# Performance work log

Measured on AMD Instinct MI355X. Metric: run time of the kernel, lower is better.

## Reference

```python
import jax, jax.numpy as jnp
import numpy as np

B_, L_, D_, N_ = 4, 4096, 64, 16
DT = 0.1
EPS = 1e-6


def _complex_log(x):
    # log|x| (clamped) + i*pi for negative entries, matching torch impl
    real = jnp.log(jnp.maximum(jnp.abs(x), EPS))
    imag = jnp.where(x < 0, jnp.float32(np.pi), jnp.float32(0.0))
    return jax.lax.complex(real, imag)


def _clogaddexp(a, b):
    # stable complex log(exp(a)+exp(b)) using max of real parts
    m = jnp.maximum(a.real, b.real)
    return jnp.log(jnp.exp(a - m) + jnp.exp(b - m)) + m


def _clogcumsumexp(x, axis):
    return jax.lax.associative_scan(_clogaddexp, x, axis=axis)


def setup_inputs() -> dict:
    key = jax.random.key(0)
    ks = jax.random.split(key, 6)
    x = jax.random.normal(ks[0], (B_, L_, D_), jnp.float32)
    s = 1.0 / np.sqrt(D_)
    Wb = jax.random.uniform(ks[1], (N_, D_), jnp.float32, -s, s)
    bb = jax.random.uniform(ks[2], (N_,), jnp.float32, -s, s)
    Wc = jax.random.uniform(ks[3], (N_, D_), jnp.float32, -s, s)
    bc = jax.random.uniform(ks[4], (N_,), jnp.float32, -s, s)
    Wd = jax.random.uniform(ks[5], (1, D_), jnp.float32, -s, s)
    bd = jnp.zeros((1,), jnp.float32)
    # S4D-Real init: A_n = -(n+1), repeated over input_dim rows -> (D, N)
    A = jnp.tile(-(jnp.arange(N_, dtype=jnp.float32) + 1.0)[None, :], (D_, 1))
    return {"x": x, "A": A, "Wb": Wb, "bb": bb, "Wc": Wc, "bc": bc,
            "Wd": Wd, "bd": bd}


def reference(x, A, Wb, bb, Wc, bc, Wd, bd):
    # projections: (b,l,n)
    Bm = x @ Wb.T + bb
    Cm = x @ Wc.T + bc
    # delta network: softplus(linear(x)) + dt, broadcast to input_dim
    delta = jax.nn.softplus(x @ Wd.T + bd) + DT            # (b,l,1)
    dt = jnp.broadcast_to(delta, x.shape)                  # (b,l,d)
    # discretize
    tmp = A * dt[..., None]                                # (b,l,d,n)
    A_bar = jnp.exp(tmp)
    delta_B = jnp.einsum('bld,bln->bldn', dt, Bm)
    B_bar = (A_bar - 1.0) * delta_B / (tmp + EPS)
    term2 = B_bar * x[..., None]                           # (b,l,d,n)
    # parallel scan via complex log-cumsum-exp trick
    log_a = _complex_log(A_bar)
    log_b = _complex_log(term2)
    a_star = jnp.cumsum(log_a, axis=1)                     # (b,l,d,n) complex
    t = _clogcumsumexp(log_b - a_star, axis=1)
    scan = jnp.exp(a_star + t).real                        # (b,l,d,n)
    return jnp.sum(scan * Cm[:, :, None, :], axis=-1)      # (b,l,d)
```

## Files before the change

### kernel.cpp

```cpp
#include <hip/hip_runtime.h>

#define B_ 4
#define L_ 4096
#define D_ 64
#define N_ 16
#define CHUNK 16
#define NCHUNK (L_ / CHUNK)
#define TOTCHUNK (B_ * NCHUNK)

constexpr float DT_  = 0.1f;
constexpr float EPS_ = 1e-6f;

__global__ __launch_bounds__(64) void proj_scan_kernel(
    const float* __restrict__ x,  const float* __restrict__ A,
    const float* __restrict__ Wb, const float* __restrict__ bb,
    const float* __restrict__ Wc, const float* __restrict__ bc,
    const float* __restrict__ Wd, const float* __restrict__ bd,
    float* __restrict__ S, float* __restrict__ Cdec,
    float* __restrict__ Wcor, float* __restrict__ out)
{
    const int gc    = blockIdx.x;
    const int batch = gc >> 8;
    const int c     = gc & (NCHUNK - 1);
    const int lane  = threadIdx.x;
    const int base0 = batch * L_ + c * CHUNK;

    __shared__ float xs[CHUNK * D_];
    __shared__ float ag[CHUNK * 32];
    __shared__ float cm[CHUNK * N_];
    __shared__ float wbuf[CHUNK * N_];

    const float4* xg  = (const float4*)(x + (size_t)base0 * D_);
    float4*       xsv = (float4*)xs;
    #pragma unroll
    for (int i = 0; i < 4; i++) xsv[i * 64 + lane] = xg[i * 64 + lane];

    const int o  = lane & 31;
    const int h2 = lane >> 5;
    float wreg[32];
    const float* Wrow = (o < 16) ? (Wb + o * D_) : (Wc + (o - 16) * D_);
    const float4* w4p = (const float4*)(Wrow + h2 * 32);
    #pragma unroll
    for (int j = 0; j < 8; j++) {
        float4 w4 = w4p[j];
        wreg[4*j+0] = w4.x; wreg[4*j+1] = w4.y;
        wreg[4*j+2] = w4.z; wreg[4*j+3] = w4.w;
    }
    const float wd   = Wd[lane];
    const float bd0  = bd[0];
    const float An   = A[lane & 15];
    const float bias = (o < 16) ? bb[o] : bc[o - 16];

    __syncthreads();

    float r[CHUNK];
    #pragma unroll
    for (int p = 0; p < CHUNK; p++) r[p] = xs[p * D_ + lane] * wd;
    #pragma unroll
    for (int m = 32; m >= 1; m >>= 1) {
        #pragma unroll
        for (int p = 0; p < CHUNK; p++) r[p] += __shfl_xor(r[p], m, 64);
    }
    float delta[CHUNK];
    #pragma unroll
    for (int p = 0; p < CHUNK; p++) {
        float z = r[p] + bd0;
        delta[p] = fmaxf(z, 0.0f) + log1pf(expf(-fabsf(z))) + DT_;
    }

    #pragma unroll
    for (int p = 0; p < CHUNK; p++) {
        float acc = 0.0f;
        const float4* xs4 = (const float4*)(xs + p * D_ + h2 * 32);
        #pragma unroll
        for (int j = 0; j < 8; j++) {
            float4 v = xs4[j];
            acc += v.x * wreg[4*j+0] + v.y * wreg[4*j+1]
                 + v.z * wreg[4*j+2] + v.w * wreg[4*j+3];
        }
        acc += __shfl_xor(acc, 32, 64);
        if (lane < 16) {
            float Bm  = acc + bias;
            float tmp = An * delta[p];
            float a   = expf(tmp);
            float g   = (a - 1.0f) * delta[p] * Bm / (tmp + EPS_);
            ag[p * 32 + lane]      = a;
            ag[p * 32 + 16 + lane] = g;
        } else if (lane < 32) {
            cm[p * 16 + (lane - 16)] = acc + bias;
        }
    }
    __syncthreads();

    float h[N_];
    #pragma unroll
    for (int n = 0; n < N_; n++) h[n] = 0.0f;
    for (int s = 0; s < CHUNK; s++) {
        float xd = xs[s * D_ + lane];
        const float4* row = (const float4*)(ag + s * 32);
        const float4* crw = (const float4*)(cm + s * 16);
        float acc = 0.0f;
        #pragma unroll
        for (int q = 0; q < 4; q++) {
            float4 a4 = row[q];
            float4 g4 = row[4 + q];
            float4 c4 = crw[q];
            h[4*q+0] = a4.x * h[4*q+0] + g4.x * xd;  acc += c4.x * h[4*q+0];
            h[4*q+1] = a4.y * h[4*q+1] + g4.y * xd;  acc += c4.y * h[4*q+1];
            h[4*q+2] = a4.z * h[4*q+2] + g4.z * xd;  acc += c4.z * h[4*q+2];
            h[4*q+3] = a4.w * h[4*q+3] + g4.w * xd;  acc += c4.w * h[4*q+3];
        }
        out[(size_t)(base0 + s) * D_ + lane] = acc;
    }
    #pragma unroll
    for (int n = 0; n < N_; n++)
        S[(size_t)(gc * N_ + n) * D_ + lane] = h[n];

    if (lane < 16) {
        float cumn = 1.0f;
        for (int s = 0; s < CHUNK; s++) {
            cumn *= ag[s * 32 + lane];
            wbuf[s * 16 + lane] = cm[s * 16 + lane] * cumn;
        }
        Cdec[gc * N_ + lane] = cumn;
    }
    __syncthreads();
    ((float4*)(Wcor + (size_t)base0 * 16))[lane] = ((const float4*)wbuf)[lane];
}

#define G_ 32
__global__ __launch_bounds__(64) void combine(
    float* __restrict__ S, const float* __restrict__ Cdec)
{
    const int b = blockIdx.x >> 4;
    const int n = blockIdx.x & 15;
    const int d = threadIdx.x;
    const int cb = b * NCHUNK;

    float*       baseS = S    + (size_t)(cb * N_ + n) * D_ + d;
    const float* baseA = Cdec + cb * N_ + n;

    float run = 0.0f;
    float sbuf[G_], abuf[G_];
    #pragma unroll
    for (int j = 0; j < G_; j++) {
        sbuf[j] = baseS[(size_t)j * (N_ * D_)];
        abuf[j] = baseA[j * N_];
    }
    for (int cc = 0; cc < NCHUNK; cc += G_) {
        const int cn = (cc + G_ < NCHUNK) ? (cc + G_) : cc;
        float t[G_], u[G_];
        #pragma unroll
        for (int j = 0; j < G_; j++) {
            t[j] = baseS[(size_t)(cn + j) * (N_ * D_)];
            u[j] = baseA[(cn + j) * N_];
        }
        #pragma unroll
        for (int j = 0; j < G_; j++) {
            baseS[(size_t)(cc + j) * (N_ * D_)] = run;
            run = abuf[j] * run + sbuf[j];
        }
        #pragma unroll
        for (int j = 0; j < G_; j++) { sbuf[j] = t[j]; abuf[j] = u[j]; }
    }
}

__global__ __launch_bounds__(64) void apply_kernel(
    const float* __restrict__ Wcor, const float* __restrict__ S,
    float* __restrict__ out)
{
    const int gc    = blockIdx.x;
    const int batch = gc >> 8;
    const int c     = gc & (NCHUNK - 1);
    const int lane  = threadIdx.x;
    const int base0 = batch * L_ + c * CHUNK;

    __shared__ float wl[CHUNK * N_];

    ((float4*)wl)[lane] = ((const float4*)(Wcor + (size_t)base0 * 16))[lane];

    float hi[N_];
    #pragma unroll
    for (int n = 0; n < N_; n++)
        hi[n] = S[(size_t)(gc * N_ + n) * D_ + lane];

    float4 ov[4];
    const float4* og = (const float4*)(out + (size_t)base0 * D_);
    #pragma unroll
    for (int i = 0; i < 4; i++) ov[i] = og[i * 64 + lane];

    __syncthreads();

    float acc[CHUNK];
    #pragma unroll
    for (int s = 0; s < CHUNK; s++) {
        const float4* crw = (const float4*)(wl + s * 16);
        float a = 0.0f;
        #pragma unroll
        for (int q = 0; q < 4; q++) {
            float4 w4 = crw[q];
            a += w4.x * hi[4*q+0] + w4.y * hi[4*q+1]
               + w4.z * hi[4*q+2] + w4.w * hi[4*q+3];
        }
        acc[s] = a;
    }

    #pragma unroll
    for (int s = 0; s < CHUNK; s++)
        out[(size_t)(base0 + s) * D_ + lane] = out[(size_t)(base0 + s) * D_ + lane] + acc[s];
}

extern "C" void kernel_launch(void* const* d_in, const int* in_sizes, int n_in,
                              void* d_out, int out_size, void* d_ws, size_t ws_size,
                              hipStream_t stream)
{
    const float* x  = (const float*)d_in[0];
    const float* A  = (const float*)d_in[1];
    const float* Wb = (const float*)d_in[2];
    const float* bb = (const float*)d_in[3];
    const float* Wc = (const float*)d_in[4];
    const float* bc = (const float*)d_in[5];
    const float* Wd = (const float*)d_in[6];
    const float* bd = (const float*)d_in[7];
    float* out = (float*)d_out;

    float* S    = (float*)d_ws;
    float* Cdec = S    + (size_t)TOTCHUNK * N_ * D_;
    float* Wcor = Cdec + (size_t)TOTCHUNK * N_;

    proj_scan_kernel<<<TOTCHUNK, 64, 0, stream>>>(x, A, Wb, bb, Wc, bc, Wd, bd,
                                                  S, Cdec, Wcor, out);
    combine<<<B_ * N_, 64, 0, stream>>>(S, Cdec);
    apply_kernel<<<TOTCHUNK, 64, 0, stream>>>(Wcor, S, out);
}
```

Before: 104.5 us.

## Split chunk work across four wavefronts per block in scan and apply kernels

Both per-chunk kernels now launch 256 threads instead of 64. In the projection/scan kernel each wavefront handles four timesteps of the projection and four of the sixteen state dimensions in the intra-chunk recurrence. Per-wave partial outputs are reduced through a new shared-memory buffer. The apply kernel also spreads timesteps across waves and folds the existing output into its accumulator. The aim is more parallelism and shorter serial chains per thread, which should help latency hiding with only 1024 blocks, at the cost of extra shared memory and a reduction pass.

New measurement: 100.3 us. 4.1% less time.

```diff
diff --git a/kernel.cpp b/kernel.cpp
--- a/kernel.cpp
+++ b/kernel.cpp
@@ -11,7 +11,7 @@
 constexpr float DT_  = 0.1f;
 constexpr float EPS_ = 1e-6f;
 
-__global__ __launch_bounds__(64) void proj_scan_kernel(
+__global__ __launch_bounds__(256) void proj_scan_kernel(
     const float* __restrict__ x,  const float* __restrict__ A,
     const float* __restrict__ Wb, const float* __restrict__ bb,
     const float* __restrict__ Wc, const float* __restrict__ bc,
@@ -22,18 +22,18 @@
     const int gc    = blockIdx.x;
     const int batch = gc >> 8;
     const int c     = gc & (NCHUNK - 1);
-    const int lane  = threadIdx.x;
+    const int tid   = threadIdx.x;
+    const int w     = tid >> 6;
+    const int lane  = tid & 63;
     const int base0 = batch * L_ + c * CHUNK;
 
     __shared__ float xs[CHUNK * D_];
     __shared__ float ag[CHUNK * 32];
     __shared__ float cm[CHUNK * N_];
     __shared__ float wbuf[CHUNK * N_];
-
-    const float4* xg  = (const float4*)(x + (size_t)base0 * D_);
-    float4*       xsv = (float4*)xs;
-    #pragma unroll
-    for (int i = 0; i < 4; i++) xsv[i * 64 + lane] = xg[i * 64 + lane];
+    __shared__ float pout[4 * CHUNK * D_];
+
+    ((float4*)xs)[tid] = ((const float4*)(x + (size_t)base0 * D_))[tid];
 
     const int o  = lane & 31;
     const int h2 = lane >> 5;
@@ -53,25 +53,27 @@
 
     __syncthreads();
 
-    float r[CHUNK];
-    #pragma unroll
-    for (int p = 0; p < CHUNK; p++) r[p] = xs[p * D_ + lane] * wd;
+    const int s0 = w * 4;
+    float r[4];
+    #pragma unroll
+    for (int p = 0; p < 4; p++) r[p] = xs[(s0 + p) * D_ + lane] * wd;
     #pragma unroll
     for (int m = 32; m >= 1; m >>= 1) {
         #pragma unroll
-        for (int p = 0; p < CHUNK; p++) r[p] += __shfl_xor(r[p], m, 64);
-    }
-    float delta[CHUNK];
-    #pragma unroll
-    for (int p = 0; p < CHUNK; p++) {
+        for (int p = 0; p < 4; p++) r[p] += __shfl_xor(r[p], m, 64);
+    }
+    float delta[4];
+    #pragma unroll
+    for (int p = 0; p < 4; p++) {
         float z = r[p] + bd0;
         delta[p] = fmaxf(z, 0.0f) + log1pf(expf(-fabsf(z))) + DT_;
     }
 
     #pragma unroll
-    for (int p = 0; p < CHUNK; p++) {
+    for (int p = 0; p < 4; p++) {
+        const int s = s0 + p;
         float acc = 0.0f;
-        const float4* xs4 = (const float4*)(xs + p * D_ + h2 * 32);
+        const float4* xs4 = (const float4*)(xs + s * D_ + h2 * 32);
         #pragma unroll
         for (int j = 0; j < 8; j++) {
             float4 v = xs4[j];
@@ -84,48 +86,53 @@
             float tmp = An * delta[p];
             float a   = expf(tmp);
             float g   = (a - 1.0f) * delta[p] * Bm / (tmp + EPS_);
-            ag[p * 32 + lane]      = a;
-            ag[p * 32 + 16 + lane] = g;
+            ag[s * 32 + lane]      = a;
+            ag[s * 32 + 16 + lane] = g;
         } else if (lane < 32) {
-            cm[p * 16 + (lane - 16)] = acc + bias;
-        }
-    }
-    __syncthreads();
-
-    float h[N_];
-    #pragma unroll
-    for (int n = 0; n < N_; n++) h[n] = 0.0f;
+            cm[s * 16 + (lane - 16)] = acc + bias;
+        }
+    }
+    __syncthreads();
+
+    const int n0 = w * 4;
+    float h0 = 0.0f, h1 = 0.0f, h2v = 0.0f, h3 = 0.0f;
+    #pragma unroll
     for (int s = 0; s < CHUNK; s++) {
-        float xd = xs[s * D_ + lane];
-        const float4* row = (const float4*)(ag + s * 32);
-        const float4* crw = (const float4*)(cm + s * 16);
-        float acc = 0.0f;
-        #pragma unroll
-        for (int q = 0; q < 4; q++) {
-            float4 a4 = row[q];
-            float4 g4 = row[4 + q];
-            float4 c4 = crw[q];
-            h[4*q+0] = a4.x * h[4*q+0] + g4.x * xd;  acc += c4.x * h[4*q+0];
-            h[4*q+1] = a4.y * h[4*q+1] + g4.y * xd;  acc += c4.y * h[4*q+1];
-            h[4*q+2] = a4.z * h[4*q+2] + g4.z * xd;  acc += c4.z * h[4*q+2];
-            h[4*q+3] = a4.w * h[4*q+3] + g4.w * xd;  acc += c4.w * h[4*q+3];
-        }
-        out[(size_t)(base0 + s) * D_ + lane] = acc;
-    }
-    #pragma unroll
-    for (int n = 0; n < N_; n++)
-        S[(size_t)(gc * N_ + n) * D_ + lane] = h[n];
-
-    if (lane < 16) {
+        float  xd = xs[s * D_ + lane];
+        float4 a4 = *(const float4*)(ag + s * 32 + n0);
+        float4 g4 = *(const float4*)(ag + s * 32 + 16 + n0);
+        float4 c4 = *(const float4*)(cm + s * 16 + n0);
+        h0 = a4.x * h0 + g4.x * xd;  float acc = c4.x * h0;
+        h1 = a4.y * h1 + g4.y * xd;  acc += c4.y * h1;
+        h2v = a4.z * h2v + g4.z * xd; acc += c4.z * h2v;
+        h3 = a4.w * h3 + g4.w * xd;  acc += c4.w * h3;
+        pout[(w * CHUNK + s) * D_ + lane] = acc;
+    }
+    S[(size_t)(gc * N_ + n0 + 0) * D_ + lane] = h0;
+    S[(size_t)(gc * N_ + n0 + 1) * D_ + lane] = h1;
+    S[(size_t)(gc * N_ + n0 + 2) * D_ + lane] = h2v;
+    S[(size_t)(gc * N_ + n0 + 3) * D_ + lane] = h3;
+
+    if (tid < 16) {
         float cumn = 1.0f;
+        #pragma unroll
         for (int s = 0; s < CHUNK; s++) {
-            cumn *= ag[s * 32 + lane];
-            wbuf[s * 16 + lane] = cm[s * 16 + lane] * cumn;
-        }
-        Cdec[gc * N_ + lane] = cumn;
-    }
-    __syncthreads();
-    ((float4*)(Wcor + (size_t)base0 * 16))[lane] = ((const float4*)wbuf)[lane];
+            cumn *= ag[s * 32 + tid];
+            wbuf[s * 16 + tid] = cm[s * 16 + tid] * cumn;
+        }
+        Cdec[gc * N_ + tid] = cumn;
+    }
+    __syncthreads();
+
+    #pragma unroll
+    for (int k = 0; k < 4; k++) {
+        const int f = k * 256 + tid;
+        float v = pout[f] + pout[CHUNK * D_ + f]
+                + pout[2 * CHUNK * D_ + f] + pout[3 * CHUNK * D_ + f];
+        out[(size_t)base0 * D_ + f] = v;
+    }
+    if (tid < 64)
+        ((float4*)(Wcor + (size_t)base0 * 16))[tid] = ((const float4*)wbuf)[tid];
 }
 
 #define G_ 32
@@ -165,49 +172,49 @@
     }
 }
 
-__global__ __launch_bounds__(64) void apply_kernel(
+__global__ __launch_bounds__(256) void apply_kernel(
     const float* __restrict__ Wcor, const float* __restrict__ S,
     float* __restrict__ out)
 {
     const int gc    = blockIdx.x;
     const int batch = gc >> 8;
     const int c     = gc & (NCHUNK - 1);
-    const int lane  = threadIdx.x;
+    const int tid   = threadIdx.x;
+    const int w     = tid >> 6;
+    const int lane  = tid & 63;
     const int base0 = batch * L_ + c * CHUNK;
 
     __shared__ float wl[CHUNK * N_];
 
-    ((float4*)wl)[lane] = ((const float4*)(Wcor + (size_t)base0 * 16))[lane];
+    if (tid < 64)
+        ((float4*)wl)[tid] = ((const float4*)(Wcor + (size_t)base0 * 16))[tid];
 
     float hi[N_];
     #pragma unroll
     for (int n = 0; n < N_; n++)
         hi[n] = S[(size_t)(gc * N_ + n) * D_ + lane];
 
-    float4 ov[4];
-    const float4* og = (const float4*)(out + (size_t)base0 * D_);
-    #pragma unroll
-    for (int i = 0; i < 4; i++) ov[i] = og[i * 64 + lane];
-
-    __syncthreads();
-
-    float acc[CHUNK];
-    #pragma unroll
-    for (int s = 0; s < CHUNK; s++) {
+    const int s0 = w * 4;
+    float oreg[4];
+    #pragma unroll
+    for (int p = 0; p < 4; p++)
+        oreg[p] = out[(size_t)(base0 + s0 + p) * D_ + lane];
+
+    __syncthreads();
+
+    #pragma unroll
+    for (int p = 0; p < 4; p++) {
+        const int s = s0 + p;
         const float4* crw = (const float4*)(wl + s * 16);
-        float a = 0.0f;
+        float a = oreg[p];
         #pragma unroll
         for (int q = 0; q < 4; q++) {
             float4 w4 = crw[q];
             a += w4.x * hi[4*q+0] + w4.y * hi[4*q+1]
                + w4.z * hi[4*q+2] + w4.w * hi[4*q+3];
         }
-        acc[s] = a;
-    }
-
-    #pragma unroll
-    for (int s = 0; s < CHUNK; s++)
-        out[(size_t)(base0 + s) * D_ + lane] = out[(size_t)(base0 + s) * D_ + lane] + acc[s];
+        out[(size_t)(base0 + s) * D_ + lane] = a;
+    }
 }
 
 extern "C" void kernel_launch(void* const* d_in, const int* in_sizes, int n_in,
@@ -228,8 +235,8 @@
     float* Cdec = S    + (size_t)TOTCHUNK * N_ * D_;
     float* Wcor = Cdec + (size_t)TOTCHUNK * N_;
 
-    proj_scan_kernel<<<TOTCHUNK, 64, 0, stream>>>(x, A, Wb, bb, Wc, bc, Wd, bd,
-                                                  S, Cdec, Wcor, out);
+    proj_scan_kernel<<<TOTCHUNK, 256, 0, stream>>>(x, A, Wb, bb, Wc, bc, Wd, bd,
+                                                   S, Cdec, Wcor, out);
     combine<<<B_ * N_, 64, 0, stream>>>(S, Cdec);
-    apply_kernel<<<TOTCHUNK, 64, 0, stream>>>(Wcor, S, out);
-}
+    apply_kernel<<<TOTCHUNK, 256, 0, stream>>>(Wcor, S, out);
+}
```
